# Kernel optimization log

Hardware: AMD Instinct MI355X
Metric: run time of the kernel (lower is better)

The kernel has to match this reference:

```python
import jax, jax.numpy as jnp
import numpy as np
from jax import lax

B, N = 16, 2048
S0, S1, K = 256, 128, 32
EPS = 1e-5


def bn_relu(x, gamma, beta, axes):
    # training-mode BatchNorm (batch statistics) + ReLU; channel is last dim
    mean = jnp.mean(x, axis=axes, keepdims=True)
    var = jnp.var(x, axis=axes, keepdims=True)
    return jax.nn.relu((x - mean) * lax.rsqrt(var + EPS) * gamma + beta)


def fps(coords, s):
    # farthest point sampling, deterministic start at index 0. coords [B,N,3]
    b, n, _ = coords.shape
    def body(carry, _):
        dist, far = carry
        centroid = jnp.take_along_axis(coords, far[:, None, None], axis=1)  # [B,1,3]
        d = jnp.sum((coords - centroid) ** 2, axis=-1)                      # [B,N]
        dist = jnp.minimum(dist, d)
        return (dist, jnp.argmax(dist, axis=-1).astype(jnp.int32)), far
    init = (jnp.full((b, n), 1e10, coords.dtype), jnp.zeros((b,), jnp.int32))
    _, idx = lax.scan(body, init, None, length=s)
    return jnp.transpose(idx)  # [B,s]


def gather_points(pts, idx):
    # pts [B,N,C], idx [B,...] int -> [B,...,C]
    flat = idx.reshape(idx.shape[0], -1)[..., None]  # [B,M,1]
    out = jnp.take_along_axis(pts, flat, axis=1)     # [B,M,C]
    return out.reshape(*idx.shape, pts.shape[-1])


def sample_and_knn_group(s, k, coords, features):
    # coords [B,N,3], features [B,N,C] -> new_xyz [B,s,3], agg [B,s,k,2C]
    fps_idx = fps(coords, s)
    new_xyz = gather_points(coords, fps_idx)      # [B,s,3]
    center = gather_points(features, fps_idx)     # [B,s,C]
    d2 = jnp.sum((new_xyz[:, :, None, :] - coords[:, None, :, :]) ** 2, axis=-1)  # [B,s,N]
    _, knn_idx = lax.top_k(-d2, k)                # k smallest distances
    grouped = gather_points(features, knn_idx)    # [B,s,k,C]
    agg = jnp.concatenate(
        [grouped - center[:, :, None, :],
         jnp.broadcast_to(center[:, :, None, :], grouped.shape)], axis=-1)
    return new_xyz, agg


def sg_block(coords, features, s, k, w, gamma, beta):
    # conv1x1 -> BN -> ReLU -> max over k neighbors
    new_xyz, nf = sample_and_knn_group(s, k, coords, features)  # nf [B,s,k,d]
    h = jnp.einsum('bskd,od->bsko', nf, w)
    h = bn_relu(h, gamma, beta, axes=(0, 1, 2))
    return new_xyz, jnp.max(h, axis=2)  # [B,s,out]


def setup_inputs() -> dict:
    key = jax.random.key(0)
    ks = jax.random.split(key, 5)
    return {
        'x': jax.random.normal(ks[0], (B, 3, N), jnp.float32),
        'w1': jax.random.normal(ks[1], (64, 3), jnp.float32) * (1.0 / np.sqrt(3)),
        'g1': jnp.ones((64,), jnp.float32), 'b1': jnp.zeros((64,), jnp.float32),
        'w2': jax.random.normal(ks[2], (64, 64), jnp.float32) * 0.125,
        'g2': jnp.ones((64,), jnp.float32), 'b2': jnp.zeros((64,), jnp.float32),
        'w_sg0': jax.random.normal(ks[3], (128, 128), jnp.float32) * (1.0 / np.sqrt(128)),
        'g_sg0': jnp.ones((128,), jnp.float32), 'b_sg0': jnp.zeros((128,), jnp.float32),
        'w_sg1': jax.random.normal(ks[4], (256, 256), jnp.float32) * (1.0 / np.sqrt(256)),
        'g_sg1': jnp.ones((256,), jnp.float32), 'b_sg1': jnp.zeros((256,), jnp.float32),
    }


def reference(x, w1, g1, b1, w2, g2, b2, w_sg0, g_sg0, b_sg0, w_sg1, g_sg1, b_sg1):
    coords = jnp.transpose(x, (0, 2, 1))                   # [B,N,3]
    f = bn_relu(jnp.einsum('bnc,oc->bno', coords, w1), g1, b1, axes=(0, 1))  # [B,N,64]
    f = bn_relu(jnp.einsum('bnc,oc->bno', f, w2), g2, b2, axes=(0, 1))       # [B,N,64]
    xyz1, f1 = sg_block(coords, f, S0, K, w_sg0, g_sg0, b_sg0)   # [B,S0,128]
    _, f2 = sg_block(xyz1, f1, S1, K, w_sg1, g_sg1, b_sg1)       # [B,S1,256]
    return jnp.transpose(f2, (0, 2, 1))                           # [B,256,S1]
```

## Files before the change

kernel.cpp:

```cpp
#include <hip/hip_runtime.h>
#include <float.h>

#define BATCH 16
#define NPTS  2048
#define NS0   256
#define NS1   128
#define KK    32
#define EPSV  1e-5f
#define MROWS 32768.0f
#define M0F   131072.0f
#define M1F   65536.0f

__device__ __forceinline__ float sqdist(float ax,float ay,float az,float bx,float by,float bz){
  float dx=__fsub_rn(ax,bx), dy=__fsub_rn(ay,by), dz=__fsub_rn(az,bz);
  return __fadd_rn(__fadd_rn(__fmul_rn(dx,dx),__fmul_rn(dy,dy)),__fmul_rn(dz,dz));
}

template<int CTRL,int RM>
__device__ __forceinline__ float dpp_fmax_s(float x){
  int t = __builtin_amdgcn_update_dpp((int)0xFF800000, __float_as_int(x), CTRL, RM, 0xf, false);
  return fmaxf(x, __int_as_float(t));
}
template<int CTRL,int RM>
__device__ __forceinline__ float dpp_fmin_s(float x){
  int t = __builtin_amdgcn_update_dpp(0x7F800000, __float_as_int(x), CTRL, RM, 0xf, false);
  return fminf(x, __int_as_float(t));
}
template<int CTRL,int RM>
__device__ __forceinline__ unsigned dpp_umin_s(unsigned x){
  unsigned t = (unsigned)__builtin_amdgcn_update_dpp(-1, (int)x, CTRL, RM, 0xf, false);
  return t<x ? t : x;
}
__device__ __forceinline__ void wave_argmax_f32(float v, unsigned idx, float& mall, int& sel){
  float m=v;
  m=dpp_fmax_s<0x111,0xf>(m); m=dpp_fmax_s<0x112,0xf>(m); m=dpp_fmax_s<0x114,0xf>(m);
  m=dpp_fmax_s<0x118,0xf>(m); m=dpp_fmax_s<0x142,0xa>(m); m=dpp_fmax_s<0x143,0xc>(m);
  mall = __int_as_float(__builtin_amdgcn_readlane(__float_as_int(m),63));
  unsigned c = (v==mall)? idx : 0xFFFFFFFFu;
  c=dpp_umin_s<0x111,0xf>(c); c=dpp_umin_s<0x112,0xf>(c); c=dpp_umin_s<0x114,0xf>(c);
  c=dpp_umin_s<0x118,0xf>(c); c=dpp_umin_s<0x142,0xa>(c); c=dpp_umin_s<0x143,0xc>(c);
  sel = (int)(unsigned)__builtin_amdgcn_readlane((int)c,63);
}
__device__ __forceinline__ int wave_argmin_f32(float v, unsigned idx){
  float m=v;
  m=dpp_fmin_s<0x111,0xf>(m); m=dpp_fmin_s<0x112,0xf>(m); m=dpp_fmin_s<0x114,0xf>(m);
  m=dpp_fmin_s<0x118,0xf>(m); m=dpp_fmin_s<0x142,0xa>(m); m=dpp_fmin_s<0x143,0xc>(m);
  float mall = __int_as_float(__builtin_amdgcn_readlane(__float_as_int(m),63));
  unsigned c = (v==mall)? idx : 0xFFFFFFFFu;
  c=dpp_umin_s<0x111,0xf>(c); c=dpp_umin_s<0x112,0xf>(c); c=dpp_umin_s<0x114,0xf>(c);
  c=dpp_umin_s<0x118,0xf>(c); c=dpp_umin_s<0x142,0xa>(c); c=dpp_umin_s<0x143,0xc>(c);
  return (int)(unsigned)__builtin_amdgcn_readlane((int)c,63);
}


__device__ void embed1_body(int bid, const float* __restrict__ x, const float* __restrict__ w1,
                            float* __restrict__ coords, float* __restrict__ t1){
  __shared__ float w[192];
  __shared__ float xs[3][64];
  __shared__ float fin[64][65];
  int tid = threadIdx.x;
  if (tid < 192) w[tid] = w1[tid];
  int base = bid*64;
  int b = base / NPTS, n0 = base % NPTS;
  if (tid < 192){
    int ch = tid>>6, i = tid&63;
    xs[ch][i] = x[((size_t)b*3+ch)*NPTS + n0 + i];
  }
  __syncthreads();
  if (tid < 64){
    coords[(size_t)(base+tid)*3+0]=xs[0][tid];
    coords[(size_t)(base+tid)*3+1]=xs[1][tid];
    coords[(size_t)(base+tid)*3+2]=xs[2][tid];
  }
  int p = tid>>2, c0 = (tid&3)<<4;
  float cx=xs[0][p], cy=xs[1][p], cz=xs[2][p];
  #pragma unroll
  for(int j=0;j<16;j++){
    int c = c0+j;
    fin[p][c] = cx*w[c*3+0] + cy*w[c*3+1] + cz*w[c*3+2];
  }
  __syncthreads();
  for(int i=tid;i<4096;i+=256){
    int pp=i>>6, c=i&63;
    t1[(size_t)base*64 + i] = fin[pp][c];
  }
}

__device__ void wt_body(int gid, const float* __restrict__ w0, float* __restrict__ wt0,
                        const float* __restrict__ w1, float* __restrict__ wt1){
  if(gid < 128*128){
    int o = gid % 128, c = gid / 128;
    wt0[gid] = w0[o*128 + c];
  } else {
    int g2 = gid - 128*128;
    if(g2 >= 256*256) return;
    int o = g2 % 256, c = g2 / 256;
    wt1[g2] = w1[o*256 + c];
  }
}

__device__ void statsA_body(int blk, const float* __restrict__ t,
                            float* __restrict__ accS, float* __restrict__ accQ){
  int c = threadIdx.x;
  int r0 = blk*128;
  float s=0.f, q=0.f;
  for(int r=0;r<128;r++){
    float v = t[(size_t)(r0+r)*64 + c];
    s+=v; q+=v*v;
  }
  atomicAdd(accS+c, s);
  atomicAdd(accQ+c, q);
}

__device__ void embed2_body(int bid, const float* __restrict__ t1, const float* __restrict__ w2,
                            const float* __restrict__ accS, const float* __restrict__ accQ,
                            const float* __restrict__ g1, const float* __restrict__ b1,
                            float* __restrict__ t2,
                            float* __restrict__ acc2S, float* __restrict__ acc2Q,
                            float* ls, float* lq, char* smem){
  float (*fin)[64] = (float(*)[64])smem;
  float* sm = (float*)smem + 4096;
  float* sr = sm+64; float* sg = sr+64; float* sb = sg+64;
  int tid = threadIdx.x;
  if (tid<64){
    float S=accS[tid], Q=accQ[tid];
    float m = S/MROWS, v = Q/MROWS - m*m; if(v<0.f) v=0.f;
    sm[tid]=m; sr[tid]=rsqrtf(v+EPSV); sg[tid]=g1[tid]; sb[tid]=b1[tid];
    ls[tid]=0.f; lq[tid]=0.f;
  }
  __syncthreads();
  int base = bid*64;
  for(int i=tid;i<4096;i+=256){
    int p=i>>6, c=i&63;
    float v = t1[(size_t)(base+p)*64 + c];
    v = (v - sm[c])*sr[c]*sg[c] + sb[c];
    fin[p][c] = v>0.f ? v : 0.f;
  }
  __syncthreads();
  int o = tid & 63, p0 = tid>>6;
  float acc[16];
  #pragma unroll
  for(int i=0;i<16;i++) acc[i]=0.f;
  for(int cc=0; cc<64; cc+=4){
    float4 wv = *(const float4*)(w2 + o*64 + cc);
    #pragma unroll
    for(int i=0;i<16;i++){
      float4 f4 = *(const float4*)&fin[p0 + i*4][cc];
      acc[i] += f4.x*wv.x + f4.y*wv.y + f4.z*wv.z + f4.w*wv.w;
    }
  }
  float s=0.f,q=0.f;
  #pragma unroll
  for(int i=0;i<16;i++){
    float v = acc[i];
    t2[(size_t)(base+p0+i*4)*64 + o] = v;
    s+=v; q+=v*v;
  }
  atomicAdd(&ls[o], s);
  atomicAdd(&lq[o], q);
  __syncthreads();
  if(tid<64){ atomicAdd(acc2S+tid, ls[tid]); atomicAdd(acc2Q+tid, lq[tid]); }
}

template<int P, int S, int T>
__device__ void fps_body(int b, const float* __restrict__ x, int* __restrict__ outIdx,
                         float* __restrict__ outXyz, char* smem){
  constexpr int PPT = P/T;
  constexpr int NW  = T/64;
  float* sx=(float*)smem; float* sy=sx+P; float* sz=sy+P;
  int* sidx=(int*)(sz+P);
  unsigned long long* rv64=(unsigned long long*)(sidx+S);
  int tid = threadIdx.x;
  const float* xb = x + (size_t)b*3*P;
  float px[PPT], py[PPT], pz[PPT], dist[PPT];
  #pragma unroll
  for(int i=0;i<PPT;i++){
    int n = i*T + tid;
    float X=xb[n], Y=xb[P+n], Z=xb[2*P+n];
    px[i]=X; py[i]=Y; pz[i]=Z; dist[i]=1e10f;
    sx[n]=X; sy[n]=Y; sz[n]=Z;
  }
  __syncthreads();
  int cur = 0;
  float cx=sx[0], cy=sy[0], cz=sz[0];
  for(int s=0;s<S;s++){
    if(tid==0) sidx[s]=cur;
    if(s==S-1) break;
    float bv=-FLT_MAX; int bi=0;
    #pragma unroll
    for(int i=0;i<PPT;i++){
      float d = sqdist(px[i],py[i],pz[i],cx,cy,cz);
      float nd = fminf(dist[i], d);
      dist[i]=nd;
      int n = i*T + tid;
      if(nd>bv){ bv=nd; bi=n; }
    }
    float mall; int sel;
    wave_argmax_f32(bv,(unsigned)bi,mall,sel);
    int sl = s & 1;
    if((tid&63)==0) rv64[sl*NW+(tid>>6)] = ((unsigned long long)__float_as_uint(mall)<<32)|(unsigned)(~sel);
    __syncthreads();
    unsigned long long wk = rv64[sl*NW];
    #pragma unroll
    for(int w=1;w<NW;w++){ unsigned long long t = rv64[sl*NW+w]; if(t>wk) wk=t; }
    cur = (int)(~(unsigned)wk);
    cx=sx[cur]; cy=sy[cur]; cz=sz[cur];
  }
  __syncthreads();
  for(int i=tid; i<S; i+=T){
    int id = sidx[i];
    outIdx[b*S+i] = id;
    outXyz[((size_t)b*S+i)*3+0] = sx[id];
    outXyz[((size_t)b*S+i)*3+1] = sy[id];
    outXyz[((size_t)b*S+i)*3+2] = sz[id];
  }
}

template<int P, int S>
__device__ void fps_wave_body(int b, const float* __restrict__ pts, int* __restrict__ outIdx,
                              float* __restrict__ outXyz, char* smem){
  constexpr int PPT = P/64;
  float4* sp = (float4*)smem;
  int* sidx = (int*)(smem + P*sizeof(float4));
  int lane = threadIdx.x;
  const float* p = pts + (size_t)b*P*3;
  float px[PPT], py[PPT], pz[PPT], dist[PPT];
  #pragma unroll
  for(int i=0;i<PPT;i++){
    int n = i*64 + lane;
    float X=p[n*3], Y=p[n*3+1], Z=p[n*3+2];
    px[i]=X; py[i]=Y; pz[i]=Z; dist[i]=1e10f;
    sp[n] = make_float4(X,Y,Z,0.f);
  }
  __syncthreads();
  int cur = 0;
  float cx=sp[0].x, cy=sp[0].y, cz=sp[0].z;
  for(int s=0;s<S;s++){
    if(lane==0) sidx[s]=cur;
    if(s==S-1) break;
    float bv=-FLT_MAX; int bi=0;
    #pragma unroll
    for(int i=0;i<PPT;i++){
      float d = sqdist(px[i],py[i],pz[i],cx,cy,cz);
      float nd = fminf(dist[i], d);
      dist[i]=nd;
      int n = i*64 + lane;
      if(nd>bv){ bv=nd; bi=n; }
    }
    float mall; int sel;
    wave_argmax_f32(bv,(unsigned)bi,mall,sel);
    cur = sel;
    float4 cp = sp[cur];
    cx=cp.x; cy=cp.y; cz=cp.z;
  }
  __syncthreads();
  for(int i=lane; i<S; i+=64){
    int id = sidx[i];
    float4 cp = sp[id];
    outIdx[b*S+i] = id;
    outXyz[((size_t)b*S+i)*3+0] = cp.x;
    outXyz[((size_t)b*S+i)*3+1] = cp.y;
    outXyz[((size_t)b*S+i)*3+2] = cp.z;
  }
}

template<int P>
__device__ void knn_compute(const float* __restrict__ p, float qx, float qy, float qz,
                            int* outRow){
  constexpr int E = P/64;
  int lane = threadIdx.x & 63;
  float dl[E];
  float b1=FLT_MAX, b2=FLT_MAX;
  unsigned i1=0xFFFFFFFFu, i2=0xFFFFFFFFu, consumed=0u;
  #pragma unroll
  for(int i=0;i<E;i++){
    unsigned n = i*64 + lane;
    float v = sqdist(qx,qy,qz,p[n*3],p[n*3+1],p[n*3+2]);
    dl[i] = v;
    bool lt1 = v<b1, lt2 = v<b2;
    float    nb2 = lt1 ? b1 : (lt2 ? v : b2);
    unsigned ni2 = lt1 ? i1 : (lt2 ? n : i2);
    b1 = lt1 ? v : b1; i1 = lt1 ? n : i1;
    b2 = nb2; i2 = ni2;
  }
  for(int j=0;j<KK;j++){
    int sel = wave_argmin_f32(b1, i1);
    if(lane==0) outRow[j] = sel;
    if((sel & 63) == lane){
      consumed |= 1u << (sel >> 6);
      b1 = b2; i1 = i2;
      b2 = FLT_MAX; i2 = 0xFFFFFFFFu;
      if(b1 == FLT_MAX){
        #pragma unroll
        for(int i=0;i<E;i++){
          float v = ((consumed>>i)&1u) ? FLT_MAX : dl[i];
          unsigned n = i*64 + lane;
          bool lt1 = v<b1, lt2 = v<b2;
          float    nb2 = lt1 ? b1 : (lt2 ? v : b2);
          unsigned ni2 = lt1 ? i1 : (lt2 ? n : i2);
          b1 = lt1 ? v : b1; i1 = lt1 ? n : i1;
          b2 = nb2; i2 = ni2;
        }
      }
    }
  }
}

template<int C, int P, int MODE>
__device__ void pass1_body(int bq, const float* __restrict__ feats, const float* __restrict__ feats2,
                           const int* knnrow, int ci, const float* __restrict__ WT,
                           float* __restrict__ hmax, float* __restrict__ hmin,
                           float* __restrict__ part, int S,
                           const float* __restrict__ accS, const float* __restrict__ accQ,
                           const float* __restrict__ bg, const float* __restrict__ bb,
                           char* smem){
  constexpr int O   = 2*C;
  constexpr int TPB = C;
  constexpr int C4  = C/4;
  constexpr int OG  = O/8;
  constexpr int LDC = C+4;
  float* gfp = (float*)smem;
  float* cf  = gfp + KK*LDC;
  float* sa  = cf + C;
  float* sbb = sa + C;
  float* sct = sbb + C;
  int tid = threadIdx.x;
  int b = bq / S;
  const float* fb = feats + (size_t)b*P*C;
  const float* fb2 = (MODE==2) ? feats2 + (size_t)b*P*C : nullptr;
  {
    float Mv = (MODE==1) ? MROWS : M0F;
    float S_=accS[tid], Q_=accQ[tid];
    float m = S_/Mv, vv = Q_/Mv - m*m; if(vv<0.f) vv=0.f;
    float a = rsqrtf(vv+EPSV)*bg[tid];
    float sh = bb[tid] - m*a;
    sa[tid]=a; sbb[tid]=sh;
    float raw;
    if(MODE==1) raw = fb[(size_t)ci*C + tid];
    else        raw = (a>=0.f) ? fb[(size_t)ci*C + tid] : fb2[(size_t)ci*C + tid];
    float cv = a*raw + sh;
    cf[tid] = cv>0.f ? cv : 0.f;
  }
  __syncthreads();
  for(int i=tid; i<KK*C4; i+=TPB){
    int k = i/C4, d4 = i - k*C4;
    size_t row = (size_t)knnrow[k]*C;
    float4 a4 = *(const float4*)&sa[d4*4];
    float4 s4 = *(const float4*)&sbb[d4*4];
    float4 c4 = *(const float4*)&cf[d4*4];
    float4 g  = ((const float4*)(fb + row))[d4];
    float4 r;
    if(MODE==2){
      float4 g2 = ((const float4*)(fb2 + row))[d4];
      float gx = (a4.x>=0.f? g.x : g2.x)*a4.x + s4.x; gx = gx>0.f?gx:0.f;
      float gy = (a4.y>=0.f? g.y : g2.y)*a4.y + s4.y; gy = gy>0.f?gy:0.f;
      float gz = (a4.z>=0.f? g.z : g2.z)*a4.z + s4.z; gz = gz>0.f?gz:0.f;
      float gw = (a4.w>=0.f? g.w : g2.w)*a4.w + s4.w; gw = gw>0.f?gw:0.f;
      r.x=gx-c4.x; r.y=gy-c4.y; r.z=gz-c4.z; r.w=gw-c4.w;
    } else {
      float gx = a4.x*g.x+s4.x; gx = gx>0.f?gx:0.f;
      float gy = a4.y*g.y+s4.y; gy = gy>0.f?gy:0.f;
      float gz = a4.z*g.z+s4.z; gz = gz>0.f?gz:0.f;
      float gw = a4.w*g.w+s4.w; gw = gw>0.f?gw:0.f;
      r.x=gx-c4.x; r.y=gy-c4.y; r.z=gz-c4.z; r.w=gw-c4.w;
    }
    *(float4*)&gfp[k*LDC + d4*4] = r;
  }
  __syncthreads();
  {
    int o2 = tid*2;
    float ct0=0.f, ct1=0.f;
    for(int c=0;c<C;c+=4){
      float4 c4 = *(const float4*)&cf[c];
      #pragma unroll
      for(int t=0;t<4;t++){
        float cv = ((const float*)&c4)[t];
        float2 wh = *(const float2*)&WT[(size_t)(C+c+t)*O + o2];
        ct0 += cv*wh.x; ct1 += cv*wh.y;
      }
    }
    sct[o2]=ct0; sct[o2+1]=ct1;
  }
  __syncthreads();
  int kg = tid / OG;
  int og = tid % OG;
  float acc[8][8];
  #pragma unroll
  for(int a=0;a<8;a++)
    #pragma unroll
    for(int bb2=0;bb2<8;bb2++) acc[a][bb2]=0.f;
  for(int dc=0; dc<C4; dc++){
    float4 g4[8];
    #pragma unroll
    for(int jk=0;jk<8;jk++) g4[jk] = *(const float4*)&gfp[(kg*8+jk)*LDC + dc*4];
    #pragma unroll
    for(int t=0;t<4;t++){
      const float* wrow = WT + (size_t)(dc*4+t)*O + og*8;
      float4 wa = *(const float4*)wrow;
      float4 wb = *(const float4*)(wrow+4);
      #pragma unroll
      for(int jk=0;jk<8;jk++){
        float gs = ((const float*)&g4[jk])[t];
        acc[jk][0] += gs*wa.x; acc[jk][1] += gs*wa.y; acc[jk][2] += gs*wa.z; acc[jk][3] += gs*wa.w;
        acc[jk][4] += gs*wb.x; acc[jk][5] += gs*wb.y; acc[jk][6] += gs*wb.z; acc[jk][7] += gs*wb.w;
      }
    }
  }
  float tmx[8],tmn[8],tsm[8],tsq[8];
  #pragma unroll
  for(int jo=0;jo<8;jo++){
    int o = og*8+jo;
    float ct = sct[o];
    float s=0.f,q=0.f,mx=-FLT_MAX,mn=FLT_MAX;
    #pragma unroll
    for(int jk=0;jk<8;jk++){
      float h = acc[jk][jo] + ct;
      s+=h; q+=h*h; mx=fmaxf(mx,h); mn=fminf(mn,h);
    }
    tmx[jo]=mx; tmn[jo]=mn; tsm[jo]=s; tsq[jo]=q;
  }
  if constexpr (TPB==64){
    #pragma unroll
    for(int jo=0;jo<8;jo++){
      tmx[jo]=fmaxf(tmx[jo],__shfl_xor(tmx[jo],16)); tmx[jo]=fmaxf(tmx[jo],__shfl_xor(tmx[jo],32));
      tmn[jo]=fminf(tmn[jo],__shfl_xor(tmn[jo],16)); tmn[jo]=fminf(tmn[jo],__shfl_xor(tmn[jo],32));
      tsm[jo]+=__shfl_xor(tsm[jo],16); tsm[jo]+=__shfl_xor(tsm[jo],32);
      tsq[jo]+=__shfl_xor(tsq[jo],16); tsq[jo]+=__shfl_xor(tsq[jo],32);
    }
    if(tid<OG){
      #pragma unroll
      for(int jo=0;jo<8;jo++){
        int o = tid*8+jo;
        hmax[(size_t)bq*O+o]=tmx[jo]; hmin[(size_t)bq*O+o]=tmn[jo];
        part[(size_t)bq*2*O+o]=tsm[jo]; part[(size_t)bq*2*O+O+o]=tsq[jo];
      }
    }
  } else {
    #pragma unroll
    for(int jo=0;jo<8;jo++){
      tmx[jo]=fmaxf(tmx[jo],__shfl_xor(tmx[jo],32));
      tmn[jo]=fminf(tmn[jo],__shfl_xor(tmn[jo],32));
      tsm[jo]+=__shfl_xor(tsm[jo],32);
      tsq[jo]+=__shfl_xor(tsq[jo],32);
    }
    int wv = tid>>6;
    if((tid&63)<32){
      int og_ = tid&31;
      size_t rb = (size_t)bq*2 + wv;
      #pragma unroll
      for(int jo=0;jo<8;jo++){
        int o = og_*8+jo;
        hmax[rb*O+o]=tmx[jo]; hmin[rb*O+o]=tmn[jo];
        part[rb*2*O+o]=tsm[jo]; part[rb*2*O+O+o]=tsq[jo];
      }
    }
  }
}


__global__ __launch_bounds__(256) void k_embed1_wt(const float* __restrict__ x, const float* __restrict__ w1,
                         float* __restrict__ coords, float* __restrict__ t1,
                         const float* __restrict__ wsg0, float* __restrict__ wt0,
                         const float* __restrict__ wsg1, float* __restrict__ wt1,
                         float* __restrict__ accz){
  if(blockIdx.x < 512) embed1_body(blockIdx.x, x, w1, coords, t1);
  else if(blockIdx.x < 832) wt_body((blockIdx.x-512)*256 + threadIdx.x, wsg0, wt0, wsg1, wt1);
  else {
    int tid = threadIdx.x;
    accz[tid]=0.f; accz[tid+256]=0.f; accz[tid+512]=0.f; accz[tid+768]=0.f;
  }
}

__global__ __launch_bounds__(64) void k_statsA(const float* __restrict__ t,
                         float* __restrict__ accS, float* __restrict__ accQ){
  statsA_body(blockIdx.x, t, accS, accQ);
}

__global__ __launch_bounds__(256, 1) void k_fps0_embed2(const float* __restrict__ x,
                         int* __restrict__ fps0, float* __restrict__ xyz0,
                         const float* __restrict__ t1, const float* __restrict__ w2,
                         const float* __restrict__ acc1S, const float* __restrict__ acc1Q,
                         const float* __restrict__ g1, const float* __restrict__ b1,
                         float* __restrict__ t2,
                         float* __restrict__ acc2S, float* __restrict__ acc2Q){
  extern __shared__ char smem[];
  __shared__ float ls[64], lq[64];
  if(blockIdx.x < BATCH) fps_body<NPTS,NS0,256>(blockIdx.x, x, fps0, xyz0, smem);
  else embed2_body(blockIdx.x-BATCH, t1, w2, acc1S, acc1Q, g1, b1, t2, acc2S, acc2Q, ls, lq, smem);
}

__global__ __launch_bounds__(64, 2) void k_fps1_p1a(const float* __restrict__ xyz0,
                         int* __restrict__ fps1, float* __restrict__ xyz1,
                         const float* __restrict__ coords, const float* __restrict__ t2,
                         const int* __restrict__ fps0, const float* __restrict__ wt0,
                         float* __restrict__ hmax0, float* __restrict__ hmin0, float* __restrict__ part0,
                         const float* __restrict__ acc2S, const float* __restrict__ acc2Q,
                         const float* __restrict__ g2, const float* __restrict__ b2){
  __shared__ __align__(16) char SU[10112];
  if(blockIdx.x < BATCH){
    fps_wave_body<NS0,NS1>(blockIdx.x, xyz0, fps1, xyz1, SU);
    return;
  }
  int bq = blockIdx.x - BATCH;
  int b = bq / NS0;
  int* sknn = (int*)(SU + 9984);
  const float* pc = coords + (size_t)b*NPTS*3;
  float qx=xyz0[(size_t)bq*3], qy=xyz0[(size_t)bq*3+1], qz=xyz0[(size_t)bq*3+2];
  knn_compute<NPTS>(pc, qx, qy, qz, sknn);
  __syncthreads();
  pass1_body<64,NPTS,1>(bq, t2, nullptr, sknn, fps0[bq], wt0, hmax0, hmin0, part0, NS0,
                        acc2S, acc2Q, g2, b2, SU);
}

__global__ __launch_bounds__(256) void k_statsB(const float* __restrict__ part, int W,
                                                float* __restrict__ acc){
  int tid = threadIdx.x;
  int r0 = blockIdx.x*64;
  for(int c=tid; c<W; c+=256){
    float a=0.f;
    for(int r=0;r<64;r++) a += part[(size_t)(r0+r)*W + c];
    atomicAdd(acc+c, a);
  }
}

__global__ __launch_bounds__(128, 2) void k_knn1_p1b(const float* __restrict__ xyz0,
                         const float* __restrict__ xyz1, const int* __restrict__ fps1,
                         const float* __restrict__ hmax0, const float* __restrict__ hmin0,
                         const float* __restrict__ wt1,
                         float* __restrict__ hmax1, float* __restrict__ hmin1, float* __restrict__ part1,
                         const float* __restrict__ accB0S, const float* __restrict__ accB0Q,
                         const float* __restrict__ gsg0, const float* __restrict__ bsg0){
  __shared__ __align__(16) char SU[19584];
  int bq = blockIdx.x;
  int b = bq / NS1;
  int* sknn = (int*)(SU + 19456);
  if(threadIdx.x < 64){
    const float* pts = xyz0 + (size_t)b*NS0*3;
    float qx=xyz1[(size_t)bq*3], qy=xyz1[(size_t)bq*3+1], qz=xyz1[(size_t)bq*3+2];
    knn_compute<NS0>(pts, qx, qy, qz, sknn);
  }
  __syncthreads();
  pass1_body<128,NS0,2>(bq, hmax0, hmin0, sknn, fps1[bq], wt1, hmax1, hmin1, part1, NS1,
                        accB0S, accB0Q, gsg0, bsg0, SU);
}

__global__ __launch_bounds__(256) void k_post1tr(const float* __restrict__ hmax, const float* __restrict__ hmin,
        const float* __restrict__ aS, const float* __restrict__ aQ,
        const float* __restrict__ g, const float* __restrict__ bb, float* __restrict__ out){
  __shared__ float ssc[64], ssh[64];
  __shared__ float tile[64][129];
  int tid = threadIdx.x;
  int blk = blockIdx.x; int b = blk>>2; int c0 = (blk&3)*64;
  if(tid<64){
    int o = c0+tid;
    float m = aS[o]/M1F, v = aQ[o]/M1F - m*m; if(v<0.f) v=0.f;
    float sc = rsqrtf(v+EPSV)*g[o];
    ssc[tid]=sc; ssh[tid]=bb[o]-m*sc;
  }
  __syncthreads();
  for(int i=tid; i<128*64; i+=256){
    int r=i>>6, ch=i&63;
    size_t rb = (size_t)(b*NS1+r)*2;
    float sc = ssc[ch];
    float va = hmax[rb*256 + c0+ch], vb = hmax[(rb+1)*256 + c0+ch];
    float wa = hmin[rb*256 + c0+ch], wb = hmin[(rb+1)*256 + c0+ch];
    float h = (sc>=0.f) ? fmaxf(va,vb) : fminf(wa,wb);
    float v = h*sc + ssh[ch];
    tile[ch][r] = v>0.f ? v : 0.f;
  }
  __syncthreads();
  for(int i=tid; i<64*128; i+=256){
    int ch=i>>7, s=i&127;
    out[(size_t)b*(256*NS1) + (size_t)(c0+ch)*NS1 + s] = tile[ch][s];
  }
}

extern "C" void kernel_launch(void* const* d_in, const int* in_sizes, int n_in,
                              void* d_out, int out_size, void* d_ws, size_t ws_size,
                              hipStream_t stream){
  const float* x    = (const float*)d_in[0];
  const float* w1   = (const float*)d_in[1];
  const float* g1   = (const float*)d_in[2];
  const float* b1   = (const float*)d_in[3];
  const float* w2   = (const float*)d_in[4];
  const float* g2   = (const float*)d_in[5];
  const float* b2   = (const float*)d_in[6];
  const float* wsg0 = (const float*)d_in[7];
  const float* gsg0 = (const float*)d_in[8];
  const float* bsg0 = (const float*)d_in[9];
  const float* wsg1 = (const float*)d_in[10];
  const float* gsg1 = (const float*)d_in[11];
  const float* bsg1 = (const float*)d_in[12];
  float* out = (float*)d_out;

  float* wsf = (float*)d_ws;
  float* coords = wsf;                    wsf += BATCH*NPTS*3;
  float* t1     = wsf;                    wsf += BATCH*NPTS*64;
  float* t2     = wsf;                    wsf += BATCH*NPTS*64;
  float* acc1S=wsf; wsf+=64;  float* acc1Q=wsf; wsf+=64;
  float* acc2S=wsf; wsf+=64;  float* acc2Q=wsf; wsf+=64;
  float* accB0=wsf; wsf+=256;
  float* accB1=wsf; wsf+=512;
  int*   fps0 = (int*)wsf;                wsf += BATCH*NS0;
  float* xyz0 = wsf;                      wsf += BATCH*NS0*3;
  float* hmax0= wsf;                      wsf += BATCH*NS0*128;
  float* hmin0= wsf;                      wsf += BATCH*NS0*128;
  float* part0= wsf;                      wsf += BATCH*NS0*2*128;
  int*   fps1 = (int*)wsf;                wsf += BATCH*NS1;
  float* xyz1 = wsf;                      wsf += BATCH*NS1*3;
  float* wt0  = wsf;                      wsf += 128*128;
  float* wt1  = wsf;                      wsf += 256*256;
  float* part1 = t1;
  float* hmax1 = t2;
  float* hmin1 = t2 + BATCH*NS1*2*256;

  const int DYN_L3 = (NPTS*3 + NS0)*4 + 2*4*8;

  k_embed1_wt<<<dim3(833), dim3(256), 0, stream>>>(x, w1, coords, t1, wsg0, wt0, wsg1, wt1, acc1S);
  k_statsA<<<dim3(256), dim3(64), 0, stream>>>(t1, acc1S, acc1Q);
  k_fps0_embed2<<<dim3(BATCH+512), dim3(256), DYN_L3, stream>>>(x, fps0, xyz0,
                                                  t1, w2, acc1S, acc1Q, g1, b1, t2, acc2S, acc2Q);
  k_fps1_p1a<<<dim3(BATCH + BATCH*NS0), dim3(64), 0, stream>>>(xyz0, fps1, xyz1,
                                                  coords, t2, fps0, wt0,
                                                  hmax0, hmin0, part0,
                                                  acc2S, acc2Q, g2, b2);
  k_statsB<<<dim3(64), dim3(256), 0, stream>>>(part0, 256, accB0);
  k_knn1_p1b<<<dim3(BATCH*NS1), dim3(128), 0, stream>>>(xyz0, xyz1, fps1,
                                                  hmax0, hmin0, wt1,
                                                  hmax1, hmin1, part1,
                                                  accB0, accB0+128, gsg0, bsg0);
  k_statsB<<<dim3(64), dim3(256), 0, stream>>>(part1, 512, accB1);
  k_post1tr<<<dim3(64), dim3(256), 0, stream>>>(hmax1, hmin1, accB1, accB1+256, gsg1, bsg1, out);
}
```

Measured before the change: 389.6 us.

## Fuse embed1 stats into embed1, single-pass 64-bit FPS argmax carrying coordinates

Computes the first BatchNorm's per-channel sum and sum of squares inside embed1 with shared-memory atomics, which removes the separate statsA kernel and its re-read of t1. Accumulator zeroing moves to a hipMemsetAsync. The FPS loop now reduces a packed 64-bit (distance, ~index) key in a single DPP pass instead of separate max and index passes. The winning lane also publishes its coordinates, so the next centroid no longer needs a dependent shared-memory lookup. The argmin helper is rewritten the same way. The trade-offs are more atomics in embed1 and wider 64-bit shuffles per DPP step.

```diff
diff --git a/kernel.cpp b/kernel.cpp
--- a/kernel.cpp
+++ b/kernel.cpp
@@ -22,11 +22,6 @@
   return fmaxf(x, __int_as_float(t));
 }
 template<int CTRL,int RM>
-__device__ __forceinline__ float dpp_fmin_s(float x){
-  int t = __builtin_amdgcn_update_dpp(0x7F800000, __float_as_int(x), CTRL, RM, 0xf, false);
-  return fminf(x, __int_as_float(t));
-}
-template<int CTRL,int RM>
 __device__ __forceinline__ unsigned dpp_umin_s(unsigned x){
   unsigned t = (unsigned)__builtin_amdgcn_update_dpp(-1, (int)x, CTRL, RM, 0xf, false);
   return t<x ? t : x;
@@ -41,23 +36,41 @@
   c=dpp_umin_s<0x118,0xf>(c); c=dpp_umin_s<0x142,0xa>(c); c=dpp_umin_s<0x143,0xc>(c);
   sel = (int)(unsigned)__builtin_amdgcn_readlane((int)c,63);
 }
+
+template<int CTRL,int RM>
+__device__ __forceinline__ unsigned long long dpp_umax64_s(unsigned long long x){
+  unsigned tlo=(unsigned)__builtin_amdgcn_update_dpp(0,(int)(unsigned)x,        CTRL,RM,0xf,false);
+  unsigned thi=(unsigned)__builtin_amdgcn_update_dpp(0,(int)(unsigned)(x>>32), CTRL,RM,0xf,false);
+  unsigned long long t=((unsigned long long)thi<<32)|tlo;
+  return t>x ? t : x;
+}
+__device__ __forceinline__ unsigned long long wave_max64(unsigned long long k){
+  k=dpp_umax64_s<0x111,0xf>(k); k=dpp_umax64_s<0x112,0xf>(k); k=dpp_umax64_s<0x114,0xf>(k);
+  k=dpp_umax64_s<0x118,0xf>(k); k=dpp_umax64_s<0x142,0xa>(k); k=dpp_umax64_s<0x143,0xc>(k);
+  return k;
+}
+template<int CTRL,int RM>
+__device__ __forceinline__ unsigned long long dpp_umin64_s(unsigned long long x){
+  unsigned tlo=(unsigned)__builtin_amdgcn_update_dpp(-1,(int)(unsigned)x,        CTRL,RM,0xf,false);
+  unsigned thi=(unsigned)__builtin_amdgcn_update_dpp(-1,(int)(unsigned)(x>>32), CTRL,RM,0xf,false);
+  unsigned long long t=((unsigned long long)thi<<32)|tlo;
+  return t<x ? t : x;
+}
 __device__ __forceinline__ int wave_argmin_f32(float v, unsigned idx){
-  float m=v;
-  m=dpp_fmin_s<0x111,0xf>(m); m=dpp_fmin_s<0x112,0xf>(m); m=dpp_fmin_s<0x114,0xf>(m);
-  m=dpp_fmin_s<0x118,0xf>(m); m=dpp_fmin_s<0x142,0xa>(m); m=dpp_fmin_s<0x143,0xc>(m);
-  float mall = __int_as_float(__builtin_amdgcn_readlane(__float_as_int(m),63));
-  unsigned c = (v==mall)? idx : 0xFFFFFFFFu;
-  c=dpp_umin_s<0x111,0xf>(c); c=dpp_umin_s<0x112,0xf>(c); c=dpp_umin_s<0x114,0xf>(c);
-  c=dpp_umin_s<0x118,0xf>(c); c=dpp_umin_s<0x142,0xa>(c); c=dpp_umin_s<0x143,0xc>(c);
-  return (int)(unsigned)__builtin_amdgcn_readlane((int)c,63);
+  unsigned long long k = ((unsigned long long)__float_as_uint(v)<<32) | (unsigned long long)idx;
+  k=dpp_umin64_s<0x111,0xf>(k); k=dpp_umin64_s<0x112,0xf>(k); k=dpp_umin64_s<0x114,0xf>(k);
+  k=dpp_umin64_s<0x118,0xf>(k); k=dpp_umin64_s<0x142,0xa>(k); k=dpp_umin64_s<0x143,0xc>(k);
+  return (int)(unsigned)__builtin_amdgcn_readlane((int)(unsigned)k,63);
 }
 
 
 __device__ void embed1_body(int bid, const float* __restrict__ x, const float* __restrict__ w1,
-                            float* __restrict__ coords, float* __restrict__ t1){
+                            float* __restrict__ coords, float* __restrict__ t1,
+                            float* __restrict__ accS, float* __restrict__ accQ){
   __shared__ float w[192];
   __shared__ float xs[3][64];
   __shared__ float fin[64][65];
+  __shared__ float ls[64], lq[64];
   int tid = threadIdx.x;
   if (tid < 192) w[tid] = w1[tid];
   int base = bid*64;
@@ -65,6 +78,9 @@
   if (tid < 192){
     int ch = tid>>6, i = tid&63;
     xs[ch][i] = x[((size_t)b*3+ch)*NPTS + n0 + i];
+  } else {
+    int t = tid - 192;
+    ls[t]=0.f; lq[t]=0.f;
   }
   __syncthreads();
   if (tid < 64){
@@ -80,10 +96,17 @@
     fin[p][c] = cx*w[c*3+0] + cy*w[c*3+1] + cz*w[c*3+2];
   }
   __syncthreads();
+  float s_=0.f, q_=0.f;
   for(int i=tid;i<4096;i+=256){
     int pp=i>>6, c=i&63;
-    t1[(size_t)base*64 + i] = fin[pp][c];
-  }
+    float v = fin[pp][c];
+    t1[(size_t)base*64 + i] = v;
+    s_+=v; q_+=v*v;
+  }
+  atomicAdd(&ls[tid&63], s_);
+  atomicAdd(&lq[tid&63], q_);
+  __syncthreads();
+  if(tid<64){ atomicAdd(accS+tid, ls[tid]); atomicAdd(accQ+tid, lq[tid]); }
 }
 
 __device__ void wt_body(int gid, const float* __restrict__ w0, float* __restrict__ wt0,
@@ -97,19 +120,6 @@
     int o = g2 % 256, c = g2 / 256;
     wt1[g2] = w1[o*256 + c];
   }
-}
-
-__device__ void statsA_body(int blk, const float* __restrict__ t,
-                            float* __restrict__ accS, float* __restrict__ accQ){
-  int c = threadIdx.x;
-  int r0 = blk*128;
-  float s=0.f, q=0.f;
-  for(int r=0;r<128;r++){
-    float v = t[(size_t)(r0+r)*64 + c];
-    s+=v; q+=v*v;
-  }
-  atomicAdd(accS+c, s);
-  atomicAdd(accQ+c, q);
 }
 
 __device__ void embed2_body(int bid, const float* __restrict__ t1, const float* __restrict__ w2,
@@ -169,7 +179,8 @@
   constexpr int NW  = T/64;
   float* sx=(float*)smem; float* sy=sx+P; float* sz=sy+P;
   int* sidx=(int*)(sz+P);
-  unsigned long long* rv64=(unsigned long long*)(sidx+S);
+  unsigned long long* rk=(unsigned long long*)(sidx+S);
+  float4* rxyz=(float4*)(rk + 2*NW);
   int tid = threadIdx.x;
   const float* xb = x + (size_t)b*3*P;
   float px[PPT], py[PPT], pz[PPT], dist[PPT];
@@ -186,25 +197,34 @@
   for(int s=0;s<S;s++){
     if(tid==0) sidx[s]=cur;
     if(s==S-1) break;
-    float bv=-FLT_MAX; int bi=0;
+    float bv=-FLT_MAX, bx=0.f, by=0.f, bz=0.f; int bi=0;
     #pragma unroll
     for(int i=0;i<PPT;i++){
       float d = sqdist(px[i],py[i],pz[i],cx,cy,cz);
       float nd = fminf(dist[i], d);
       dist[i]=nd;
-      int n = i*T + tid;
-      if(nd>bv){ bv=nd; bi=n; }
-    }
-    float mall; int sel;
-    wave_argmax_f32(bv,(unsigned)bi,mall,sel);
+      bool g = nd>bv;
+      bv = g?nd:bv; bi = g?(i*T+tid):bi;
+      bx = g?px[i]:bx; by = g?py[i]:by; bz = g?pz[i]:bz;
+    }
+    unsigned long long key = ((unsigned long long)__float_as_uint(bv)<<32) | (unsigned)~(unsigned)bi;
+    unsigned long long red = wave_max64(key);
+    int sel = (int)~(unsigned)__builtin_amdgcn_readlane((int)(unsigned)red, 63);
     int sl = s & 1;
-    if((tid&63)==0) rv64[sl*NW+(tid>>6)] = ((unsigned long long)__float_as_uint(mall)<<32)|(unsigned)(~sel);
+    if((tid&63) == (sel&63)){
+      int w = tid>>6;
+      rk[sl*NW+w]   = key;
+      rxyz[sl*NW+w] = make_float4(bx,by,bz,0.f);
+    }
     __syncthreads();
-    unsigned long long wk = rv64[sl*NW];
-    #pragma unroll
-    for(int w=1;w<NW;w++){ unsigned long long t = rv64[sl*NW+w]; if(t>wk) wk=t; }
+    unsigned long long wk = rk[sl*NW]; float4 cp = rxyz[sl*NW];
+    #pragma unroll
+    for(int w=1;w<NW;w++){
+      unsigned long long t = rk[sl*NW+w]; float4 tp = rxyz[sl*NW+w];
+      if(t>wk){ wk=t; cp=tp; }
+    }
     cur = (int)(~(unsigned)wk);
-    cx=sx[cur]; cy=sy[cur]; cz=sz[cur];
+    cx=cp.x; cy=cp.y; cz=cp.z;
   }
   __syncthreads();
   for(int i=tid; i<S; i+=T){
@@ -462,18 +482,9 @@
                          float* __restrict__ coords, float* __restrict__ t1,
                          const float* __restrict__ wsg0, float* __restrict__ wt0,
                          const float* __restrict__ wsg1, float* __restrict__ wt1,
-                         float* __restrict__ accz){
-  if(blockIdx.x < 512) embed1_body(blockIdx.x, x, w1, coords, t1);
-  else if(blockIdx.x < 832) wt_body((blockIdx.x-512)*256 + threadIdx.x, wsg0, wt0, wsg1, wt1);
-  else {
-    int tid = threadIdx.x;
-    accz[tid]=0.f; accz[tid+256]=0.f; accz[tid+512]=0.f; accz[tid+768]=0.f;
-  }
-}
-
-__global__ __launch_bounds__(64) void k_statsA(const float* __restrict__ t,
-                         float* __restrict__ accS, float* __restrict__ accQ){
-  statsA_body(blockIdx.x, t, accS, accQ);
+                         float* __restrict__ acc1S, float* __restrict__ acc1Q){
+  if(blockIdx.x < 512) embed1_body(blockIdx.x, x, w1, coords, t1, acc1S, acc1Q);
+  else wt_body((blockIdx.x-512)*256 + threadIdx.x, wsg0, wt0, wsg1, wt1);
 }
 
 __global__ __launch_bounds__(256, 1) void k_fps0_embed2(const float* __restrict__ x,
@@ -614,10 +625,11 @@
   float* hmax1 = t2;
   float* hmin1 = t2 + BATCH*NS1*2*256;
 
-  const int DYN_L3 = (NPTS*3 + NS0)*4 + 2*4*8;
-
-  k_embed1_wt<<<dim3(833), dim3(256), 0, stream>>>(x, w1, coords, t1, wsg0, wt0, wsg1, wt1, acc1S);
-  k_statsA<<<dim3(256), dim3(64), 0, stream>>>(t1, acc1S, acc1Q);
+  const int DYN_L3 = (NPTS*3 + NS0)*4 + 2*4*8 + 2*4*16;
+
+  hipMemsetAsync(acc1S, 0, 1024*sizeof(float), stream);
+  k_embed1_wt<<<dim3(832), dim3(256), 0, stream>>>(x, w1, coords, t1, wsg0, wt0, wsg1, wt1,
+                                                   acc1S, acc1Q);
   k_fps0_embed2<<<dim3(BATCH+512), dim3(256), DYN_L3, stream>>>(x, fps0, xyz0,
                                                   t1, w2, acc1S, acc1Q, g1, b1, t2, acc2S, acc2Q);
   k_fps1_p1a<<<dim3(BATCH + BATCH*NS0), dim3(64), 0, stream>>>(xyz0, fps1, xyz1,
```

Result: slower. 421.0 us (+8.1%).
